# Performance work log

Hardware: AMD Instinct MI355X
Metric: run time of the kernel (lower is better)

Reference implementation:

```python
import jax, jax.numpy as jnp
import numpy as np

TOP_K = 32
SCALE_FACTOR = 8.0
NEG_INF = -1e18


def setup_inputs() -> dict:
    key = jax.random.key(0)
    kq, kk, kv = jax.random.split(key, 3)
    B, H, S, D = 2, 16, 2048, 64
    q = jax.random.normal(kq, (B, H, S, D), dtype=jnp.float32)
    k = jax.random.normal(kk, (B, H, S, D), dtype=jnp.float32)
    v = jax.random.normal(kv, (B, H, S, D), dtype=jnp.float32)
    return {"q": q, "k": k, "v": v}


def reference(q, k, v):
    # scores: [B, H, Sq, Sk]
    scores = jnp.einsum("bhqd,bhkd->bhqk", q, k) / SCALE_FACTOR
    # torch code clamps top_k against key.size()[-1] == head dim D (quirk);
    # with TOP_K=32 < D=64 the clamp is inactive.
    top_k = min(TOP_K, k.shape[-1])
    topv, _ = jax.lax.top_k(scores, top_k)            # [B,H,Sq,top_k], sorted desc
    thresh = topv[..., -1:]                            # k-th largest per query row
    mask_k = scores < thresh                           # True -> masked out
    scores = jnp.where(mask_k, NEG_INF, scores)
    attn = jax.nn.softmax(scores, axis=-1)
    context = jnp.einsum("bhqk,bhkd->bhqd", attn, v)
    return context, attn, mask_k
```

## Files before the change

### kernel.cpp

```cpp
#include <hip/hip_runtime.h>
#include <math.h>

namespace {
constexpr int kS = 2048;
constexpr int kD = 64;
constexpr int kBH = 32;
constexpr int kTopK = 32;
constexpr int kPadBins = 2112;
constexpr int kCandCap = 128;
constexpr int kKeepCap = 64;
constexpr size_t kCtxElems  = (size_t)kBH * kS * kD;
constexpr size_t kAttnElems = (size_t)kBH * kS * kS;
}

typedef float f2 __attribute__((ext_vector_type(2)));

__device__ __forceinline__ unsigned sortable_bits(float x) {
  unsigned u = __float_as_uint(x);
  return u ^ ((u & 0x80000000u) ? 0xFFFFFFFFu : 0x80000000u);
}

__global__ __launch_bounds__(256) void qk_scores(const float* __restrict__ q,
                                                 const float* __restrict__ k,
                                                 float* __restrict__ scores) {
  __shared__ float QsT[32][132];
  __shared__ float KsT[32][132];
  const int bh  = blockIdx.z;
  const int q0  = blockIdx.y * 128;
  const int k0  = blockIdx.x * 128;
  const int tid = threadIdx.x;
  const float* qg = q + ((size_t)bh * kS + q0) * kD;
  const float* kg = k + ((size_t)bh * kS + k0) * kD;

  const int ty8 = (tid >> 4) * 8;
  const int tx8 = (tid & 15) * 8;
  f2 acc[8][4] = {};

  for (int half = 0; half < 2; ++half) {
    if (half) __syncthreads();
#pragma unroll
    for (int rnd = 0; rnd < 4; ++rnd) {
      int flat = rnd * 1024 + tid * 4;
      int r = flat >> 5;
      int c = flat & 31;
      float4 qv = *(const float4*)(qg + r * kD + half * 32 + c);
      QsT[c + 0][r] = qv.x;
      QsT[c + 1][r] = qv.y;
      QsT[c + 2][r] = qv.z;
      QsT[c + 3][r] = qv.w;
      float4 kv = *(const float4*)(kg + r * kD + half * 32 + c);
      KsT[c + 0][r] = kv.x;
      KsT[c + 1][r] = kv.y;
      KsT[c + 2][r] = kv.z;
      KsT[c + 3][r] = kv.w;
    }
    __syncthreads();

#pragma unroll
    for (int kk = 0; kk < 32; ++kk) {
      float a[8];
      f2 b[4];
      *(float4*)(&a[0]) = *(const float4*)(&QsT[kk][ty8]);
      *(float4*)(&a[4]) = *(const float4*)(&QsT[kk][ty8 + 4]);
      float4 b0 = *(const float4*)(&KsT[kk][tx8]);
      float4 b1 = *(const float4*)(&KsT[kk][tx8 + 4]);
      b[0] = f2{b0.x, b0.y};
      b[1] = f2{b0.z, b0.w};
      b[2] = f2{b1.x, b1.y};
      b[3] = f2{b1.z, b1.w};
#pragma unroll
      for (int i = 0; i < 8; ++i) {
        const f2 as = {a[i], a[i]};
#pragma unroll
        for (int j2 = 0; j2 < 4; ++j2)
          acc[i][j2] += as * b[j2];
      }
    }
  }

#pragma unroll
  for (int i = 0; i < 8; ++i) {
    float* orow = scores + ((size_t)bh * kS + q0 + ty8 + i) * kS + k0 + tx8;
    float4 o0 = make_float4(acc[i][0].x * 0.125f, acc[i][0].y * 0.125f,
                            acc[i][1].x * 0.125f, acc[i][1].y * 0.125f);
    float4 o1 = make_float4(acc[i][2].x * 0.125f, acc[i][2].y * 0.125f,
                            acc[i][3].x * 0.125f, acc[i][3].y * 0.125f);
    *(float4*)(orow)     = o0;
    *(float4*)(orow + 4) = o1;
  }
}

__global__ __launch_bounds__(256) void topk_softmax(const float* __restrict__ v,
                                                    float* __restrict__ ctx,
                                                    float* __restrict__ attn,
                                                    float* __restrict__ mask) {
  __shared__ unsigned s_hist[4][kPadBins];
  __shared__ float    s_cand[4][kCandCap];
  __shared__ int      s_kidx[4][kKeepCap];
  __shared__ float    s_kw[4][kKeepCap];
  __shared__ unsigned s_nc[4];

  const int tid  = threadIdx.x;
  const int wid  = tid >> 6;
  const int lane = tid & 63;
  const int row  = blockIdx.x * 4 + wid;
  const int bh   = row >> 11;
  unsigned* hist = s_hist[wid];

  const float* srow = attn + (size_t)row * kS;
  float locv[32];
#pragma unroll
  for (int g = 0; g < 8; ++g)
    *(float4*)(&locv[g * 4]) = *(const float4*)(srow + g * 256 + lane * 4);

#pragma unroll
  for (int j = 0; j < 33; ++j) hist[j * 64 + lane] = 0u;
  if (lane == 0) s_nc[wid] = 0u;

  float pmax = locv[0];
#pragma unroll
  for (int j = 0; j < 32; ++j) {
    unsigned b = sortable_bits(locv[j]) >> 21;
    atomicAdd(&hist[b + (b >> 5)], 1u);
    pmax = fmaxf(pmax, locv[j]);
  }
#pragma unroll
  for (int off = 32; off >= 1; off >>= 1)
    pmax = fmaxf(pmax, __shfl_xor(pmax, off));

  asm volatile("s_waitcnt lgkmcnt(0)" ::: "memory");

  unsigned lsum = 0;
#pragma unroll
  for (int j = 0; j < 32; ++j) lsum += hist[lane * 33 + j];
  unsigned sfx = lsum;
#pragma unroll
  for (int off = 1; off < 64; off <<= 1) {
    unsigned z = __shfl_down(sfx, off);
    if (lane + off < 64) sfx += z;
  }
  const unsigned above = sfx - lsum;

  int bstar = 0, gabove = 0;
  const bool ispiv = (sfx >= (unsigned)kTopK) && (above < (unsigned)kTopK);
  if (ispiv) {
    unsigned run = above;
    for (int j = 31; j >= 0; --j) {
      unsigned h = hist[lane * 33 + j];
      if (run < (unsigned)kTopK && run + h >= (unsigned)kTopK) {
        bstar  = lane * 32 + j;
        gabove = (int)run;
      }
      run += h;
    }
  }
  const unsigned long long pm = __ballot(ispiv);
  const int psrc = __ffsll(pm) - 1;
  bstar  = __shfl(bstar, psrc);
  gabove = __shfl(gabove, psrc);

#pragma unroll
  for (int j = 0; j < 32; ++j) {
    unsigned b = sortable_bits(locv[j]) >> 21;
    if ((int)b == bstar) {
      unsigned p = atomicAdd(&s_nc[wid], 1u);
      if (p < (unsigned)kCandCap) s_cand[wid][p] = locv[j];
    }
  }
  asm volatile("s_waitcnt lgkmcnt(0)" ::: "memory");
  const int m = (int)min(s_nc[wid], (unsigned)kCandCap);

  const float x0 = (lane < m) ? s_cand[wid][lane] : 0.0f;
  const float x1 = (lane + 64 < m) ? s_cand[wid][lane + 64] : 0.0f;
  int g0 = 0, e0 = 0, g1 = 0, e1 = 0;
  for (int j = 0; j < m; ++j) {
    float y = s_cand[wid][j];
    g0 += (y > x0); e0 += (y == x0);
    g1 += (y > x1); e1 += (y == x1);
  }
  const bool win0 = (lane < m) &&
                    (gabove + g0 < kTopK) && (gabove + g0 + e0 >= kTopK);
  const bool win1 = (lane + 64 < m) &&
                    (gabove + g1 < kTopK) && (gabove + g1 + e1 >= kTopK);
  const unsigned long long wm0 = __ballot(win0);
  const unsigned long long wm1 = __ballot(win1);
  float t32;
  if (wm0 != 0ull)      t32 = __shfl(x0, __ffsll(wm0) - 1);
  else if (wm1 != 0ull) t32 = __shfl(x1, __ffsll(wm1) - 1);
  else                  t32 = pmax;

  const unsigned long long below = (1ull << lane) - 1ull;
  float w32[32];
  float psum = 0.0f;
  int nkbase = 0;
#pragma unroll
  for (int j = 0; j < 32; ++j) {
    const bool keep = (locv[j] >= t32);
    const float wv = keep ? __expf(locv[j] - pmax) : 0.0f;
    w32[j] = wv;
    psum += wv;
    const unsigned long long mk = __ballot(keep);
    if (keep) {
      const int slot = nkbase + (int)__popcll(mk & below);
      if (slot < kKeepCap) {
        s_kidx[wid][slot] = (j >> 2) * 256 + lane * 4 + (j & 3);
        s_kw[wid][slot]   = wv;
      }
    }
    nkbase += (int)__popcll(mk);
  }
  const int nk = nkbase < kKeepCap ? nkbase : kKeepCap;
#pragma unroll
  for (int off = 32; off >= 1; off >>= 1)
    psum += __shfl_xor(psum, off);
  const float invZ = 1.0f / psum;

  float* arow = attn + (size_t)row * kS;
  float* mrow = mask + (size_t)row * kS;
#pragma unroll
  for (int g = 0; g < 8; ++g) {
    float4 a = make_float4(w32[g*4+0] * invZ, w32[g*4+1] * invZ,
                           w32[g*4+2] * invZ, w32[g*4+3] * invZ);
    float4 mm = make_float4(locv[g*4+0] >= t32 ? 0.f : 1.f,
                            locv[g*4+1] >= t32 ? 0.f : 1.f,
                            locv[g*4+2] >= t32 ? 0.f : 1.f,
                            locv[g*4+3] >= t32 ? 0.f : 1.f);
    *(float4*)(arow + g * 256 + lane * 4) = a;
    *(float4*)(mrow + g * 256 + lane * 4) = mm;
  }

  asm volatile("s_waitcnt lgkmcnt(0)" ::: "memory");
  const float* vb = v + ((size_t)bh * kS) * kD + lane;
  float acc = 0.0f;
  int c = 0;
  for (; c + 8 <= nk; c += 8) {
    float w[8], vv[8];
    int   ii[8];
#pragma unroll
    for (int u = 0; u < 8; ++u) {
      w[u]  = s_kw[wid][c + u];
      ii[u] = s_kidx[wid][c + u];
    }
#pragma unroll
    for (int u = 0; u < 8; ++u)
      vv[u] = vb[(size_t)ii[u] * kD];
#pragma unroll
    for (int u = 0; u < 8; ++u)
      acc += w[u] * vv[u];
  }
  for (; c < nk; ++c)
    acc += s_kw[wid][c] * vb[(size_t)s_kidx[wid][c] * kD];
  ctx[(size_t)row * kD + lane] = acc * invZ;
}

extern "C" void kernel_launch(void* const* d_in, const int* in_sizes, int n_in,
                              void* d_out, int out_size, void* d_ws, size_t ws_size,
                              hipStream_t stream) {
  const float* q = (const float*)d_in[0];
  const float* k = (const float*)d_in[1];
  const float* v = (const float*)d_in[2];
  float* out  = (float*)d_out;
  float* ctx  = out;
  float* attn = out + kCtxElems;
  float* mask = attn + kAttnElems;

  dim3 g1(kS / 128, kS / 128, kBH);
  qk_scores<<<g1, 256, 0, stream>>>(q, k, attn);
  topk_softmax<<<dim3(kBH * kS / 4), 256, 0, stream>>>(v, ctx, attn, mask);
}
```

Measured before the change: 1.374 ms.

## Pack histogram bins as 16-bit pairs and recompute weights to raise occupancy

The per-wave radix histogram now stores two 16-bit bin counters per 32-bit LDS word, roughly halving histogram shared memory. The 32-element weight array is dropped, and exp values are recomputed in the output store loop to cut register pressure. Launch bounds request 5 blocks per SM. Together these aim to raise occupancy of the memory-bound top-k/softmax kernel, at the cost of a second exp pass and extra shift/mask work on histogram reads.

Result: slower. 1.536 ms (+11.8%).

```diff
diff --git a/kernel.cpp b/kernel.cpp
--- a/kernel.cpp
+++ b/kernel.cpp
@@ -6,7 +6,7 @@
 constexpr int kD = 64;
 constexpr int kBH = 32;
 constexpr int kTopK = 32;
-constexpr int kPadBins = 2112;
+constexpr int kPadWords = 1088;
 constexpr int kCandCap = 128;
 constexpr int kKeepCap = 64;
 constexpr size_t kCtxElems  = (size_t)kBH * kS * kD;
@@ -90,11 +90,11 @@
   }
 }
 
-__global__ __launch_bounds__(256) void topk_softmax(const float* __restrict__ v,
-                                                    float* __restrict__ ctx,
-                                                    float* __restrict__ attn,
-                                                    float* __restrict__ mask) {
-  __shared__ unsigned s_hist[4][kPadBins];
+__global__ __launch_bounds__(256, 5) void topk_softmax(const float* __restrict__ v,
+                                                       float* __restrict__ ctx,
+                                                       float* __restrict__ attn,
+                                                       float* __restrict__ mask) {
+  __shared__ unsigned s_hist[4][kPadWords];
   __shared__ float    s_cand[4][kCandCap];
   __shared__ int      s_kidx[4][kKeepCap];
   __shared__ float    s_kw[4][kKeepCap];
@@ -114,14 +114,15 @@
     *(float4*)(&locv[g * 4]) = *(const float4*)(srow + g * 256 + lane * 4);
 
 #pragma unroll
-  for (int j = 0; j < 33; ++j) hist[j * 64 + lane] = 0u;
+  for (int j = 0; j < 17; ++j) hist[j * 64 + lane] = 0u;
   if (lane == 0) s_nc[wid] = 0u;
 
   float pmax = locv[0];
 #pragma unroll
   for (int j = 0; j < 32; ++j) {
     unsigned b = sortable_bits(locv[j]) >> 21;
-    atomicAdd(&hist[b + (b >> 5)], 1u);
+    unsigned w = b >> 1;
+    atomicAdd(&hist[w + (w >> 4)], 1u << ((b & 1) << 4));
     pmax = fmaxf(pmax, locv[j]);
   }
 #pragma unroll
@@ -132,7 +133,10 @@
 
   unsigned lsum = 0;
 #pragma unroll
-  for (int j = 0; j < 32; ++j) lsum += hist[lane * 33 + j];
+  for (int jw = 0; jw < 16; ++jw) {
+    unsigned w = hist[lane * 17 + jw];
+    lsum += (w & 0xFFFFu) + (w >> 16);
+  }
   unsigned sfx = lsum;
 #pragma unroll
   for (int off = 1; off < 64; off <<= 1) {
@@ -146,7 +150,8 @@
   if (ispiv) {
     unsigned run = above;
     for (int j = 31; j >= 0; --j) {
-      unsigned h = hist[lane * 33 + j];
+      unsigned wv = hist[lane * 17 + (j >> 1)];
+      unsigned h = (wv >> ((j & 1) << 4)) & 0xFFFFu;
       if (run < (unsigned)kTopK && run + h >= (unsigned)kTopK) {
         bstar  = lane * 32 + j;
         gabove = (int)run;
@@ -190,14 +195,12 @@
   else                  t32 = pmax;
 
   const unsigned long long below = (1ull << lane) - 1ull;
-  float w32[32];
   float psum = 0.0f;
   int nkbase = 0;
 #pragma unroll
   for (int j = 0; j < 32; ++j) {
     const bool keep = (locv[j] >= t32);
     const float wv = keep ? __expf(locv[j] - pmax) : 0.0f;
-    w32[j] = wv;
     psum += wv;
     const unsigned long long mk = __ballot(keep);
     if (keep) {
@@ -219,14 +222,16 @@
   float* mrow = mask + (size_t)row * kS;
 #pragma unroll
   for (int g = 0; g < 8; ++g) {
-    float4 a = make_float4(w32[g*4+0] * invZ, w32[g*4+1] * invZ,
-                           w32[g*4+2] * invZ, w32[g*4+3] * invZ);
-    float4 mm = make_float4(locv[g*4+0] >= t32 ? 0.f : 1.f,
-                            locv[g*4+1] >= t32 ? 0.f : 1.f,
-                            locv[g*4+2] >= t32 ? 0.f : 1.f,
-                            locv[g*4+3] >= t32 ? 0.f : 1.f);
-    *(float4*)(arow + g * 256 + lane * 4) = a;
-    *(float4*)(mrow + g * 256 + lane * 4) = mm;
+    float aw[4], mw[4];
+#pragma unroll
+    for (int u = 0; u < 4; ++u) {
+      const float x = locv[g * 4 + u];
+      const bool keep = (x >= t32);
+      aw[u] = (keep ? __expf(x - pmax) : 0.0f) * invZ;
+      mw[u] = keep ? 0.f : 1.f;
+    }
+    *(float4*)(arow + g * 256 + lane * 4) = make_float4(aw[0], aw[1], aw[2], aw[3]);
+    *(float4*)(mrow + g * 256 + lane * 4) = make_float4(mw[0], mw[1], mw[2], mw[3]);
   }
 
   asm volatile("s_waitcnt lgkmcnt(0)" ::: "memory");
```

## Replace LDS histogram top-k threshold with ballot-based bisection on sortable bits

Applied to the files above, without the earlier changes.

The top-k threshold search no longer builds a 2048-bin shared-memory histogram with atomics. It bisects over the sortable-bit value range, counting elements at or above the midpoint with wave ballots and popcounts, until at most 96 candidates remain or the interval collapses. The remaining candidates are then compacted into shared memory without atomics and ranked as before. This removes the LDS atomic traffic and the histogram clearing, and frees shared memory for occupancy, but each bisection step costs 32 ballots and the number of iterations depends on the data, possibly up to about 32.

Measured after the change: 1.380 ms. No clear change (+0.4%).

```diff
diff --git a/kernel.cpp b/kernel.cpp
--- a/kernel.cpp
+++ b/kernel.cpp
@@ -6,7 +6,6 @@
 constexpr int kD = 64;
 constexpr int kBH = 32;
 constexpr int kTopK = 32;
-constexpr int kPadBins = 2112;
 constexpr int kCandCap = 128;
 constexpr int kKeepCap = 64;
 constexpr size_t kCtxElems  = (size_t)kBH * kS * kD;
@@ -18,6 +17,10 @@
 __device__ __forceinline__ unsigned sortable_bits(float x) {
   unsigned u = __float_as_uint(x);
   return u ^ ((u & 0x80000000u) ? 0xFFFFFFFFu : 0x80000000u);
+}
+
+__device__ __forceinline__ float unsortable_float(unsigned s) {
+  return __uint_as_float(s ^ ((s & 0x80000000u) ? 0x80000000u : 0xFFFFFFFFu));
 }
 
 __global__ __launch_bounds__(256) void qk_scores(const float* __restrict__ q,
@@ -94,18 +97,15 @@
                                                     float* __restrict__ ctx,
                                                     float* __restrict__ attn,
                                                     float* __restrict__ mask) {
-  __shared__ unsigned s_hist[4][kPadBins];
   __shared__ float    s_cand[4][kCandCap];
   __shared__ int      s_kidx[4][kKeepCap];
   __shared__ float    s_kw[4][kKeepCap];
-  __shared__ unsigned s_nc[4];
 
   const int tid  = threadIdx.x;
   const int wid  = tid >> 6;
   const int lane = tid & 63;
   const int row  = blockIdx.x * 4 + wid;
   const int bh   = row >> 11;
-  unsigned* hist = s_hist[wid];
 
   const float* srow = attn + (size_t)row * kS;
   float locv[32];
@@ -113,83 +113,65 @@
   for (int g = 0; g < 8; ++g)
     *(float4*)(&locv[g * 4]) = *(const float4*)(srow + g * 256 + lane * 4);
 
-#pragma unroll
-  for (int j = 0; j < 33; ++j) hist[j * 64 + lane] = 0u;
-  if (lane == 0) s_nc[wid] = 0u;
+  const unsigned long long below = (1ull << lane) - 1ull;
 
   float pmax = locv[0];
 #pragma unroll
-  for (int j = 0; j < 32; ++j) {
-    unsigned b = sortable_bits(locv[j]) >> 21;
-    atomicAdd(&hist[b + (b >> 5)], 1u);
-    pmax = fmaxf(pmax, locv[j]);
-  }
+  for (int j = 0; j < 32; ++j) pmax = fmaxf(pmax, locv[j]);
 #pragma unroll
   for (int off = 32; off >= 1; off >>= 1)
     pmax = fmaxf(pmax, __shfl_xor(pmax, off));
 
-  asm volatile("s_waitcnt lgkmcnt(0)" ::: "memory");
-
-  unsigned lsum = 0;
-#pragma unroll
-  for (int j = 0; j < 32; ++j) lsum += hist[lane * 33 + j];
-  unsigned sfx = lsum;
-#pragma unroll
-  for (int off = 1; off < 64; off <<= 1) {
-    unsigned z = __shfl_down(sfx, off);
-    if (lane + off < 64) sfx += z;
-  }
-  const unsigned above = sfx - lsum;
-
-  int bstar = 0, gabove = 0;
-  const bool ispiv = (sfx >= (unsigned)kTopK) && (above < (unsigned)kTopK);
-  if (ispiv) {
-    unsigned run = above;
-    for (int j = 31; j >= 0; --j) {
-      unsigned h = hist[lane * 33 + j];
-      if (run < (unsigned)kTopK && run + h >= (unsigned)kTopK) {
-        bstar  = lane * 32 + j;
-        gabove = (int)run;
-      }
-      run += h;
-    }
-  }
-  const unsigned long long pm = __ballot(ispiv);
-  const int psrc = __ffsll(pm) - 1;
-  bstar  = __shfl(bstar, psrc);
-  gabove = __shfl(gabove, psrc);
-
-#pragma unroll
-  for (int j = 0; j < 32; ++j) {
-    unsigned b = sortable_bits(locv[j]) >> 21;
-    if ((int)b == bstar) {
-      unsigned p = atomicAdd(&s_nc[wid], 1u);
-      if (p < (unsigned)kCandCap) s_cand[wid][p] = locv[j];
-    }
-  }
-  asm volatile("s_waitcnt lgkmcnt(0)" ::: "memory");
-  const int m = (int)min(s_nc[wid], (unsigned)kCandCap);
-
-  const float x0 = (lane < m) ? s_cand[wid][lane] : 0.0f;
-  const float x1 = (lane + 64 < m) ? s_cand[wid][lane + 64] : 0.0f;
-  int g0 = 0, e0 = 0, g1 = 0, e1 = 0;
-  for (int j = 0; j < m; ++j) {
-    float y = s_cand[wid][j];
-    g0 += (y > x0); e0 += (y == x0);
-    g1 += (y > x1); e1 += (y == x1);
-  }
-  const bool win0 = (lane < m) &&
-                    (gabove + g0 < kTopK) && (gabove + g0 + e0 >= kTopK);
-  const bool win1 = (lane + 64 < m) &&
-                    (gabove + g1 < kTopK) && (gabove + g1 + e1 >= kTopK);
-  const unsigned long long wm0 = __ballot(win0);
-  const unsigned long long wm1 = __ballot(win1);
+  unsigned lo = 0u, hi = sortable_bits(pmax) + 1u;
+  int cnt_lo = kS, cnt_hi = 0;
+  while ((cnt_lo - cnt_hi > 96) && (hi - lo > 1u)) {
+    const unsigned mid = lo + ((hi - lo) >> 1);
+    const float fmid = unsortable_float(mid);
+    int c = 0;
+#pragma unroll
+    for (int j = 0; j < 32; ++j)
+      c += (int)__popcll(__ballot(locv[j] >= fmid));
+    if (c >= kTopK) { lo = mid; cnt_lo = c; }
+    else            { hi = mid; cnt_hi = c; }
+  }
+  const float flo = unsortable_float(lo);
+  const float fhi = unsortable_float(hi);
+
   float t32;
-  if (wm0 != 0ull)      t32 = __shfl(x0, __ffsll(wm0) - 1);
-  else if (wm1 != 0ull) t32 = __shfl(x1, __ffsll(wm1) - 1);
-  else                  t32 = pmax;
-
-  const unsigned long long below = (1ull << lane) - 1ull;
+  if (hi - lo == 1u) {
+    t32 = flo;
+  } else {
+    int nc = 0;
+#pragma unroll
+    for (int j = 0; j < 32; ++j) {
+      const bool in = (locv[j] >= flo) && (locv[j] < fhi);
+      const unsigned long long mk = __ballot(in);
+      if (in) s_cand[wid][nc + (int)__popcll(mk & below)] = locv[j];
+      nc += (int)__popcll(mk);
+    }
+    asm volatile("s_waitcnt lgkmcnt(0)" ::: "memory");
+    const int m = nc;
+    const int gabove = cnt_hi;
+
+    const float x0 = (lane < m) ? s_cand[wid][lane] : 0.0f;
+    const float x1 = (lane + 64 < m) ? s_cand[wid][lane + 64] : 0.0f;
+    int g0 = 0, e0 = 0, g1 = 0, e1 = 0;
+    for (int j = 0; j < m; ++j) {
+      float y = s_cand[wid][j];
+      g0 += (y > x0); e0 += (y == x0);
+      g1 += (y > x1); e1 += (y == x1);
+    }
+    const bool win0 = (lane < m) &&
+                      (gabove + g0 < kTopK) && (gabove + g0 + e0 >= kTopK);
+    const bool win1 = (lane + 64 < m) &&
+                      (gabove + g1 < kTopK) && (gabove + g1 + e1 >= kTopK);
+    const unsigned long long wm0 = __ballot(win0);
+    const unsigned long long wm1 = __ballot(win1);
+    if (wm0 != 0ull)      t32 = __shfl(x0, __ffsll(wm0) - 1);
+    else if (wm1 != 0ull) t32 = __shfl(x1, __ffsll(wm1) - 1);
+    else                  t32 = pmax;
+  }
+
   float w32[32];
   float psum = 0.0f;
   int nkbase = 0;
```
